# Performance work log

Hardware: AMD Instinct MI355X
Metric: run time of the kernel (lower is better)

The kernel has to match this reference:

```python
import jax, jax.numpy as jnp
import numpy as np

N_HEADS = 4
NUM_GROUPS = 32
EPS = 1e-6


def _nin(t, W, b):
    # 1x1 conv as dense over channel dim: [B,C,H,W] x [C,D] -> [B,D,H,W]
    return jnp.einsum('bchw,cd->bdhw', t, W) + b[None, :, None, None]


def setup_inputs() -> dict:
    key = jax.random.key(0)
    ks = jax.random.split(key, 12)
    B, C, H, W = 8, 256, 32, 32
    Tc = 512
    Cin = C + Tc  # 768
    x = jax.random.normal(ks[0], (B, C, H, W), dtype=jnp.float32)
    text_feat = jax.random.normal(ks[1], (B, Tc), dtype=jnp.float32)
    gn_gamma = jnp.ones((Cin,), dtype=jnp.float32)
    gn_beta = jnp.zeros((Cin,), dtype=jnp.float32)
    scale = 1.0 / np.sqrt(Cin)
    W0 = jax.random.normal(ks[2], (Cin, C), dtype=jnp.float32) * scale
    b0 = jnp.zeros((C,), dtype=jnp.float32)
    W1 = jax.random.normal(ks[3], (Cin, C), dtype=jnp.float32) * scale
    b1 = jnp.zeros((C,), dtype=jnp.float32)
    W2 = jax.random.normal(ks[4], (Cin, C), dtype=jnp.float32) * scale
    b2 = jnp.zeros((C,), dtype=jnp.float32)
    return {"x": x, "text_feat": text_feat, "gn_gamma": gn_gamma, "gn_beta": gn_beta,
            "W0": W0, "b0": b0, "W1": W1, "b1": b1, "W2": W2, "b2": b2}


def reference(x, text_feat, gn_gamma, gn_beta, W0, b0, W1, b1, W2, b2):
    B, C, H, W = x.shape
    # broadcast text features spatially and concat on channel dim
    tf = jnp.broadcast_to(text_feat[:, :, None, None], (B, text_feat.shape[1], H, W))
    h = jnp.concatenate([x, tf], axis=1)  # [B, C+Tc, H, W]
    Ctot = h.shape[1]
    # GroupNorm(32, Ctot), eps=1e-6
    hg = h.reshape(B, NUM_GROUPS, Ctot // NUM_GROUPS, H, W)
    mu = hg.mean(axis=(2, 3, 4), keepdims=True)
    var = hg.var(axis=(2, 3, 4), keepdims=True)
    hn = ((hg - mu) * jax.lax.rsqrt(var + EPS)).reshape(B, Ctot, H, W)
    hn = hn * gn_gamma[None, :, None, None] + gn_beta[None, :, None, None]
    q = _nin(hn, W0, b0)
    k = _nin(hn, W1, b1)
    v = _nin(hn, W2, b2)
    Ch = C // N_HEADS
    qh = q.reshape(B * N_HEADS, Ch, H, W)
    kh = k.reshape(B * N_HEADS, Ch, H, W)
    vh = v.reshape(B * N_HEADS, Ch, H, W)
    # full HW x HW attention scores, softmax over flattened key positions
    w = jnp.einsum('bchw,bcij->bhwij', qh, kh) * (Ch ** -0.5)
    w = jax.nn.softmax(w.reshape(B * N_HEADS, H, W, H * W), axis=-1)
    w = w.reshape(B * N_HEADS, H, W, H, W)
    ho = jnp.einsum('bhwij,bcij->bchw', w, vh).reshape(B, C, H, W)
    return x + ho
```

## Files before the change

### kernel.cpp

```cpp
#include <hip/hip_runtime.h>
#include <math.h>

#define BATCH 8
#define CX 256
#define TC 512
#define CIN 768
#define HW_TOT 1024
#define NH 4
#define CHD 64

typedef __attribute__((ext_vector_type(8))) short short8;
typedef __attribute__((ext_vector_type(4))) short s4v;
typedef __attribute__((ext_vector_type(4))) float floatx4;
typedef __attribute__((ext_vector_type(4))) int int4v;

#define QSCALE 0.18033688f

static __device__ __forceinline__ short f2bf(float f) {
    union { float f; unsigned u; } c; c.f = f;
    unsigned r = (c.u + 0x7fffu + ((c.u >> 16) & 1u)) >> 16;
    return (short)r;
}

static __device__ __forceinline__ int pack_trunc(float lo, float hi) {
    union { float f; unsigned u; } L, H;
    L.f = lo; H.f = hi;
    return (int)((H.u & 0xffff0000u) | (L.u >> 16));
}

__global__ __launch_bounds__(256)
void gn_kernel(const float* __restrict__ x, const float* __restrict__ tf,
               const float* __restrict__ gamma, const float* __restrict__ beta,
               float* __restrict__ scale, float* __restrict__ shift,
               float* __restrict__ tc) {
    const int b = blockIdx.x >> 5;
    const int g = blockIdx.x & 31;
    const int t = threadIdx.x;
    const int w = t >> 6, lane = t & 63;
    if (blockIdx.x < 24) tc[blockIdx.x * 256 + t] = 0.f;

    float s = 0.f, ss = 0.f;
    #pragma unroll
    for (int rr = 0; rr < 6; rr++) {
        const int row = w * 6 + rr;
        const int cg = g * 24 + row;
        if (cg < CX) {
            const float4* p = (const float4*)(x + ((size_t)b * CX + cg) * HW_TOT);
            #pragma unroll
            for (int i = 0; i < 4; i++) {
                float4 v = p[lane + 64 * i];
                s += v.x + v.y + v.z + v.w;
                ss += v.x * v.x + v.y * v.y + v.z * v.z + v.w * v.w;
            }
        } else {
            float v = tf[b * TC + cg - CX];
            s += 16.f * v;
            ss += 16.f * v * v;
        }
    }
    #pragma unroll
    for (int d = 1; d < 64; d <<= 1) {
        s += __shfl_xor(s, d);
        ss += __shfl_xor(ss, d);
    }
    __shared__ float rs_[4], rss_[4];
    if (lane == 0) { rs_[w] = s; rss_[w] = ss; }
    __syncthreads();
    const float S  = rs_[0] + rs_[1] + rs_[2] + rs_[3];
    const float SS = rss_[0] + rss_[1] + rss_[2] + rss_[3];
    const float inv_n = 1.f / (24 * 1024);
    const float mean = S * inv_n;
    const float var = SS * inv_n - mean * mean;
    const float r = rsqrtf(var + 1e-6f);
    if (t < 24) {
        int cg = g * 24 + t;
        float sc = gamma[cg] * r;
        scale[b * CIN + cg] = sc;
        shift[b * CIN + cg] = beta[cg] - mean * sc;
    }
}

__global__ __launch_bounds__(256)
void prep_kernel(const float* __restrict__ x, const float* __restrict__ tf,
                 const float* __restrict__ scale, const float* __restrict__ shift,
                 const float* __restrict__ W0, const float* __restrict__ W1,
                 const float* __restrict__ W2,
                 short* __restrict__ hnT, short* __restrict__ Wt,
                 float* __restrict__ tc) {
    __shared__ float hs[128];
    __shared__ float red[4][64];
    const int bx = blockIdx.x;
    const int t = threadIdx.x;
    if (bx < 256) {
        int id = (bx & 31) * 256 + t;
        int b = id >> 10;
        const float* xb = x + (size_t)b * CX * HW_TOT + (id & 1023);
        const float* scb = scale + b * CIN;
        const float* shb = shift + b * CIN;
        short* outp = hnT + (size_t)id * CX;
        int c0base = (bx >> 5) * 32;
        for (int c0 = c0base; c0 < c0base + 32; c0 += 8) {
            short8 o;
            #pragma unroll
            for (int i = 0; i < 8; i++) {
                float v = xb[(size_t)(c0 + i) * HW_TOT];
                o[i] = f2bf(v * scb[c0 + i] + shb[c0 + i]);
            }
            *(short8*)(outp + c0) = o;
        }
    } else if (bx < 268) {
        int m = bx - 256;
        int dg = (m % 3) * 256 + t;
        int which = dg >> 8, d = dg & 255;
        const float* Wm = (which == 0) ? W0 : (which == 1) ? W1 : W2;
        int c0base = (m / 3) * 64;
        for (int c0 = c0base; c0 < c0base + 64; c0 += 8) {
            short8 o;
            #pragma unroll
            for (int i = 0; i < 8; i++) o[i] = f2bf(Wm[(size_t)(c0 + i) * CX + d]);
            *(short8*)(Wt + (size_t)dg * CX + c0) = o;
        }
    } else {
        int m = bx - 268;
        int ks = m & 3;
        int b = (m >> 2) & 7, dt = m >> 5;
        int which = dt >> 2, d0 = (dt & 3) * 64;
        const float* Wm = (which == 0) ? W0 : (which == 1) ? W1 : W2;
        if (t < 128) {
            int c = ks * 128 + t;
            hs[t] = tf[b * TC + c] * scale[b * CIN + CX + c] + shift[b * CIN + CX + c];
        }
        __syncthreads();
        int td = t & 63, tq = t >> 6;
        float acc = 0.f;
        const float* wp = Wm + (size_t)(CX + ks * 128 + tq * 32) * CX + d0 + td;
        #pragma unroll 8
        for (int c = 0; c < 32; c++)
            acc = fmaf(hs[tq * 32 + c], wp[(size_t)c * CX], acc);
        red[tq][td] = acc;
        __syncthreads();
        if (t < 64)
            atomicAdd(&tc[b * CIN + which * CX + d0 + t],
                      red[0][t] + red[1][t] + red[2][t] + red[3][t]);
    }
}

__global__ __launch_bounds__(256)
void qkv_gemm(const short* __restrict__ hnT, const short* __restrict__ Wt,
              const float* __restrict__ tc,
              const float* __restrict__ b0, const float* __restrict__ b1,
              const float* __restrict__ b2,
              short* __restrict__ qb, short* __restrict__ kb, short* __restrict__ vb) {
    const int hw0 = blockIdx.x * 64, dt = blockIdx.y, b = blockIdx.z;
    const int which = dt >> 2;
    const int col0 = (dt & 3) * 64;
    const int dg0 = which * 256 + col0;
    const bool OV = (which == 2);

    __shared__ short At[64 * 72];
    __shared__ short Bt[64 * 72];

    const int t = threadIdx.x;
    const int w = t >> 6, l = t & 63;
    const int wm = w >> 1, wn = w & 1;
    const int l15 = l & 15, q = l >> 4;
    const int srow = t >> 2, sch = (t & 3) * 16;

    const short* gA = hnT + (size_t)(b * HW_TOT + hw0 + srow) * CX + sch;
    const short* gB = Wt + (size_t)(dg0 + srow) * CX + sch;

    floatx4 acc[2][2] = {};
    for (int k0 = 0; k0 < CX; k0 += 64) {
        __syncthreads();
        *(short8*)(At + srow * 72 + sch)     = *(const short8*)(gA + k0);
        *(short8*)(At + srow * 72 + sch + 8) = *(const short8*)(gA + k0 + 8);
        *(short8*)(Bt + srow * 72 + sch)     = *(const short8*)(gB + k0);
        *(short8*)(Bt + srow * 72 + sch + 8) = *(const short8*)(gB + k0 + 8);
        __syncthreads();
        const short* aB = OV ? Bt : At;
        const short* bB = OV ? At : Bt;
        #pragma unroll
        for (int kc = 0; kc < 2; kc++) {
            short8 af[2], bf2[2];
            #pragma unroll
            for (int mt = 0; mt < 2; mt++)
                af[mt] = *(const short8*)(aB + (wm * 32 + mt * 16 + l15) * 72 + kc * 32 + q * 8);
            #pragma unroll
            for (int nt = 0; nt < 2; nt++)
                bf2[nt] = *(const short8*)(bB + (wn * 32 + nt * 16 + l15) * 72 + kc * 32 + q * 8);
            #pragma unroll
            for (int mt = 0; mt < 2; mt++)
                #pragma unroll
                for (int nt = 0; nt < 2; nt++)
                    acc[mt][nt] = __builtin_amdgcn_mfma_f32_16x16x32_bf16(
                        af[mt], bf2[nt], acc[mt][nt], 0, 0, 0);
        }
    }

    __syncthreads();
    const float* bias = (which == 0) ? b0 : (which == 1) ? b1 : b2;
    if (!OV) {
        const float qs = (which == 0) ? QSCALE : 1.0f;
        float cadd[2];
        #pragma unroll
        for (int nt = 0; nt < 2; nt++) {
            int d = col0 + wn * 32 + nt * 16 + l15;
            cadd[nt] = bias[d] + tc[b * CIN + which * CX + d];
        }
        #pragma unroll
        for (int mt = 0; mt < 2; mt++)
            #pragma unroll
            for (int rr = 0; rr < 4; rr++)
                #pragma unroll
                for (int nt = 0; nt < 2; nt++)
                    At[(wm * 32 + mt * 16 + q * 4 + rr) * 72 + wn * 32 + nt * 16 + l15]
                        = f2bf((acc[mt][nt][rr] + cadd[nt]) * qs);
    } else {
        #pragma unroll
        for (int mt = 0; mt < 2; mt++)
            #pragma unroll
            for (int rr = 0; rr < 4; rr++) {
                int d = col0 + wm * 32 + mt * 16 + q * 4 + rr;
                float radd = bias[d] + tc[b * CIN + 2 * CX + d];
                #pragma unroll
                for (int nt = 0; nt < 2; nt++)
                    At[(wm * 32 + mt * 16 + q * 4 + rr) * 72 + wn * 32 + nt * 16 + l15]
                        = f2bf(acc[mt][nt][rr] + radd);
            }
    }
    __syncthreads();
    short8 v0 = *(const short8*)(At + srow * 72 + sch);
    short8 v1 = *(const short8*)(At + srow * 72 + sch + 8);
    if (!OV) {
        short* outp = (which == 0) ? qb : kb;
        size_t off = (size_t)(b * HW_TOT + hw0 + srow) * CX + col0 + sch;
        *(short8*)(outp + off) = v0;
        *(short8*)(outp + off + 8) = v1;
    } else {
        size_t off = (size_t)(b * CX + col0 + srow) * HW_TOT + hw0 + sch;
        *(short8*)(vb + off) = v0;
        *(short8*)(vb + off + 8) = v1;
    }
}

__global__ __launch_bounds__(256)
void attn_kernel(const short* __restrict__ qb, const short* __restrict__ kb,
                 const short* __restrict__ vb, const float* __restrict__ x,
                 float* __restrict__ out) {
    const int qt = blockIdx.x, bh = blockIdx.y;
    const int b = bh >> 2, h = bh & 3;
    const int hw0 = qt * 128;

    __shared__ short Qs[128 * 72];
    __shared__ short Ks[2][64 * 72];
    __shared__ short Vs[2][64 * 72];

    const int t = threadIdx.x;
    const int w = t >> 6, l = t & 63;
    const int l15 = l & 15, q = l >> 4;
    const int srow = t >> 2, sch = (t & 3) * 16;
    const int vpos0 = ((sch >> 5) << 5) + ((sch >> 4) & 1) * 4;

    {
        #pragma unroll
        for (int rr = 0; rr < 2; rr++) {
            const short* gq = qb + (size_t)(b * HW_TOT + hw0 + rr * 64 + srow) * CX
                            + h * CHD + sch;
            *(short8*)(Qs + (rr * 64 + srow) * 72 + sch)     = *(const short8*)gq;
            *(short8*)(Qs + (rr * 64 + srow) * 72 + sch + 8) = *(const short8*)(gq + 8);
        }
    }

    short8 pk0, pk1, pv0, pv1;
    {
        const short* gk = kb + (size_t)(b * HW_TOT + 0 + srow) * CX + h * CHD + sch;
        pk0 = *(const short8*)gk;
        pk1 = *(const short8*)(gk + 8);
        const short* gv = vb + (size_t)(b * CX + h * CHD + srow) * HW_TOT + 0 + sch;
        pv0 = *(const short8*)gv;
        pv1 = *(const short8*)(gv + 8);
        *(short8*)(Ks[0] + srow * 72 + sch)     = pk0;
        *(short8*)(Ks[0] + srow * 72 + sch + 8) = pk1;
        short* vrow = Vs[0] + srow * 72 + vpos0;
        *(s4v*)(vrow)      = __builtin_shufflevector(pv0, pv0, 0, 1, 2, 3);
        *(s4v*)(vrow + 8)  = __builtin_shufflevector(pv0, pv0, 4, 5, 6, 7);
        *(s4v*)(vrow + 16) = __builtin_shufflevector(pv1, pv1, 0, 1, 2, 3);
        *(s4v*)(vrow + 24) = __builtin_shufflevector(pv1, pv1, 4, 5, 6, 7);
    }
    __syncthreads();

    short8 aq[2][2];
    #pragma unroll
    for (int g = 0; g < 2; g++) {
        aq[g][0] = *(const short8*)(Qs + (w * 32 + g * 16 + l15) * 72 + q * 8);
        aq[g][1] = *(const short8*)(Qs + (w * 32 + g * 16 + l15) * 72 + 32 + q * 8);
    }

    union { int4v i; short8 s; } ones;
    ones.i[0] = 0x3f803f80; ones.i[1] = 0x3f803f80;
    ones.i[2] = 0x3f803f80; ones.i[3] = 0x3f803f80;

    floatx4 oacc[2][4] = {};
    floatx4 lacc[2] = {};

    for (int jj = 0; jj < 16; jj++) {
        const int cur = jj & 1;
        if (jj < 15) {
            const int j0 = (jj + 1) * 64;
            const short* gk = kb + (size_t)(b * HW_TOT + j0 + srow) * CX + h * CHD + sch;
            pk0 = *(const short8*)gk;
            pk1 = *(const short8*)(gk + 8);
            const short* gv = vb + (size_t)(b * CX + h * CHD + srow) * HW_TOT + j0 + sch;
            pv0 = *(const short8*)gv;
            pv1 = *(const short8*)(gv + 8);
        }

        const short* Kc = Ks[cur];
        floatx4 sacc[2][4] = {};
        #pragma unroll
        for (int nt = 0; nt < 4; nt++) {
            short8 kf0 = *(const short8*)(Kc + (nt * 16 + l15) * 72 + q * 8);
            short8 kf1 = *(const short8*)(Kc + (nt * 16 + l15) * 72 + 32 + q * 8);
            #pragma unroll
            for (int g = 0; g < 2; g++) {
                sacc[g][nt] = __builtin_amdgcn_mfma_f32_16x16x32_bf16(kf0, aq[g][0], sacc[g][nt], 0, 0, 0);
                sacc[g][nt] = __builtin_amdgcn_mfma_f32_16x16x32_bf16(kf1, aq[g][1], sacc[g][nt], 0, 0, 0);
            }
        }

        union { int4v i; short8 s; } u[2][2];
        #pragma unroll
        for (int g = 0; g < 2; g++)
            #pragma unroll
            for (int nt = 0; nt < 4; nt++) {
                float e0 = exp2f(sacc[g][nt][0]);
                float e1 = exp2f(sacc[g][nt][1]);
                float e2 = exp2f(sacc[g][nt][2]);
                float e3 = exp2f(sacc[g][nt][3]);
                u[g][nt >> 1].i[(nt & 1) * 2]     = pack_trunc(e0, e1);
                u[g][nt >> 1].i[(nt & 1) * 2 + 1] = pack_trunc(e2, e3);
            }

        #pragma unroll
        for (int g = 0; g < 2; g++) {
            lacc[g] = __builtin_amdgcn_mfma_f32_16x16x32_bf16(ones.s, u[g][0].s, lacc[g], 0, 0, 0);
            lacc[g] = __builtin_amdgcn_mfma_f32_16x16x32_bf16(ones.s, u[g][1].s, lacc[g], 0, 0, 0);
        }

        const short* Vc = Vs[cur];
        #pragma unroll
        for (int ct = 0; ct < 4; ct++) {
            const short* vr = Vc + (ct * 16 + l15) * 72;
            #pragma unroll
            for (int kcc = 0; kcc < 2; kcc++) {
                short8 vf = *(const short8*)(vr + kcc * 32 + q * 8);
                #pragma unroll
                for (int g = 0; g < 2; g++)
                    oacc[g][ct] = __builtin_amdgcn_mfma_f32_16x16x32_bf16(
                        vf, u[g][kcc].s, oacc[g][ct], 0, 0, 0);
            }
        }

        if (jj < 15) {
            __syncthreads();
            *(short8*)(Ks[1 - cur] + srow * 72 + sch)     = pk0;
            *(short8*)(Ks[1 - cur] + srow * 72 + sch + 8) = pk1;
            short* vrow = Vs[1 - cur] + srow * 72 + vpos0;
            *(s4v*)(vrow)      = __builtin_shufflevector(pv0, pv0, 0, 1, 2, 3);
            *(s4v*)(vrow + 8)  = __builtin_shufflevector(pv0, pv0, 4, 5, 6, 7);
            *(s4v*)(vrow + 16) = __builtin_shufflevector(pv1, pv1, 0, 1, 2, 3);
            *(s4v*)(vrow + 24) = __builtin_shufflevector(pv1, pv1, 4, 5, 6, 7);
            __syncthreads();
        }
    }

    #pragma unroll
    for (int g = 0; g < 2; g++) {
        const float rinv = 1.f / lacc[g][0];
        #pragma unroll
        for (int ct = 0; ct < 4; ct++)
            #pragma unroll
            for (int r = 0; r < 4; r++) {
                int c = h * CHD + ct * 16 + q * 4 + r;
                size_t idx = (size_t)(b * CX + c) * HW_TOT + hw0 + w * 32 + g * 16 + l15;
                out[idx] = x[idx] + oacc[g][ct][r] * rinv;
            }
    }
}

extern "C" void kernel_launch(void* const* d_in, const int* in_sizes, int n_in,
                              void* d_out, int out_size, void* d_ws, size_t ws_size,
                              hipStream_t stream) {
    (void)in_sizes; (void)n_in; (void)out_size; (void)ws_size;
    const float* x     = (const float*)d_in[0];
    const float* tf    = (const float*)d_in[1];
    const float* gamma = (const float*)d_in[2];
    const float* beta  = (const float*)d_in[3];
    const float* W0 = (const float*)d_in[4];
    const float* b0 = (const float*)d_in[5];
    const float* W1 = (const float*)d_in[6];
    const float* b1 = (const float*)d_in[7];
    const float* W2 = (const float*)d_in[8];
    const float* b2 = (const float*)d_in[9];

    char* ws = (char*)d_ws;
    float* scale  = (float*)(ws);
    float* shift  = (float*)(ws + 24576);
    float* tcb    = (float*)(ws + 49152);
    short* Wt     = (short*)(ws + 73728);
    short* hnT    = (short*)(ws + 466944);
    short* qb     = (short*)(ws + 4661248);
    short* kb     = (short*)(ws + 8855552);
    short* vb     = (short*)(ws + 13049856);

    hipLaunchKernelGGL(gn_kernel, dim3(256), dim3(256), 0, stream,
                       x, tf, gamma, beta, scale, shift, tcb);
    hipLaunchKernelGGL(prep_kernel, dim3(652), dim3(256), 0, stream,
                       x, tf, scale, shift, W0, W1, W2, hnT, Wt, tcb);
    hipLaunchKernelGGL(qkv_gemm, dim3(16, 12, BATCH), dim3(256), 0, stream,
                       hnT, Wt, tcb, b0, b1, b2, qb, kb, vb);
    hipLaunchKernelGGL(attn_kernel, dim3(8, 32), dim3(256), 0, stream,
                       qb, kb, vb, x, (float*)d_out);
}
```

Measured before the change: 124.9 us.

## Split attention key range across wave pairs and halve query tile per block

The attention kernel now handles 64 queries per block instead of 128, which doubles the grid to 512 blocks. Within a block, two wave pairs each process one half of the key sequence (a split-K style scheme) and merge their partial outputs and row sums through shared memory at the end. The intent is more blocks and more parallelism to fill the CUs, plus a launch-bounds occupancy hint. The cost is a doubled K/V load per query, with each K/V tile now read by twice as many blocks, and an extra shared-memory reduction. Dropping the per-tile double buffering also exposes some load latency.

```diff
diff --git a/kernel.cpp b/kernel.cpp
--- a/kernel.cpp
+++ b/kernel.cpp
@@ -243,57 +243,59 @@
     }
 }
 
-__global__ __launch_bounds__(256)
+__global__ __launch_bounds__(256, 3)
 void attn_kernel(const short* __restrict__ qb, const short* __restrict__ kb,
                  const short* __restrict__ vb, const float* __restrict__ x,
                  float* __restrict__ out) {
     const int qt = blockIdx.x, bh = blockIdx.y;
     const int b = bh >> 2, h = bh & 3;
-    const int hw0 = qt * 128;
-
-    __shared__ short Qs[128 * 72];
+    const int hw0 = qt * 64;
+
+    __shared__ short Qs[64 * 72];
     __shared__ short Ks[2][64 * 72];
     __shared__ short Vs[2][64 * 72];
 
     const int t = threadIdx.x;
     const int w = t >> 6, l = t & 63;
+    const int pair = w >> 1, jh = w & 1;
     const int l15 = l & 15, q = l >> 4;
     const int srow = t >> 2, sch = (t & 3) * 16;
     const int vpos0 = ((sch >> 5) << 5) + ((sch >> 4) & 1) * 4;
 
     {
-        #pragma unroll
-        for (int rr = 0; rr < 2; rr++) {
-            const short* gq = qb + (size_t)(b * HW_TOT + hw0 + rr * 64 + srow) * CX
-                            + h * CHD + sch;
-            *(short8*)(Qs + (rr * 64 + srow) * 72 + sch)     = *(const short8*)gq;
-            *(short8*)(Qs + (rr * 64 + srow) * 72 + sch + 8) = *(const short8*)(gq + 8);
-        }
-    }
-
-    short8 pk0, pk1, pv0, pv1;
-    {
-        const short* gk = kb + (size_t)(b * HW_TOT + 0 + srow) * CX + h * CHD + sch;
-        pk0 = *(const short8*)gk;
-        pk1 = *(const short8*)(gk + 8);
-        const short* gv = vb + (size_t)(b * CX + h * CHD + srow) * HW_TOT + 0 + sch;
-        pv0 = *(const short8*)gv;
-        pv1 = *(const short8*)(gv + 8);
-        *(short8*)(Ks[0] + srow * 72 + sch)     = pk0;
-        *(short8*)(Ks[0] + srow * 72 + sch + 8) = pk1;
-        short* vrow = Vs[0] + srow * 72 + vpos0;
-        *(s4v*)(vrow)      = __builtin_shufflevector(pv0, pv0, 0, 1, 2, 3);
-        *(s4v*)(vrow + 8)  = __builtin_shufflevector(pv0, pv0, 4, 5, 6, 7);
-        *(s4v*)(vrow + 16) = __builtin_shufflevector(pv1, pv1, 0, 1, 2, 3);
-        *(s4v*)(vrow + 24) = __builtin_shufflevector(pv1, pv1, 4, 5, 6, 7);
+        const short* gq = qb + (size_t)(b * HW_TOT + hw0 + srow) * CX + h * CHD + sch;
+        *(short8*)(Qs + srow * 72 + sch)     = *(const short8*)gq;
+        *(short8*)(Qs + srow * 72 + sch + 8) = *(const short8*)(gq + 8);
+    }
+
+    short8 pk[2][2], pv[2][2];
+    #pragma unroll
+    for (int s = 0; s < 2; s++) {
+        const int j0 = s * 512;
+        const short* gk = kb + (size_t)(b * HW_TOT + j0 + srow) * CX + h * CHD + sch;
+        pk[s][0] = *(const short8*)gk;
+        pk[s][1] = *(const short8*)(gk + 8);
+        const short* gv = vb + (size_t)(b * CX + h * CHD + srow) * HW_TOT + j0 + sch;
+        pv[s][0] = *(const short8*)gv;
+        pv[s][1] = *(const short8*)(gv + 8);
+    }
+    #pragma unroll
+    for (int s = 0; s < 2; s++) {
+        *(short8*)(Ks[s] + srow * 72 + sch)     = pk[s][0];
+        *(short8*)(Ks[s] + srow * 72 + sch + 8) = pk[s][1];
+        short* vrow = Vs[s] + srow * 72 + vpos0;
+        *(s4v*)(vrow)      = __builtin_shufflevector(pv[s][0], pv[s][0], 0, 1, 2, 3);
+        *(s4v*)(vrow + 8)  = __builtin_shufflevector(pv[s][0], pv[s][0], 4, 5, 6, 7);
+        *(s4v*)(vrow + 16) = __builtin_shufflevector(pv[s][1], pv[s][1], 0, 1, 2, 3);
+        *(s4v*)(vrow + 24) = __builtin_shufflevector(pv[s][1], pv[s][1], 4, 5, 6, 7);
     }
     __syncthreads();
 
     short8 aq[2][2];
     #pragma unroll
     for (int g = 0; g < 2; g++) {
-        aq[g][0] = *(const short8*)(Qs + (w * 32 + g * 16 + l15) * 72 + q * 8);
-        aq[g][1] = *(const short8*)(Qs + (w * 32 + g * 16 + l15) * 72 + 32 + q * 8);
+        aq[g][0] = *(const short8*)(Qs + (pair * 32 + g * 16 + l15) * 72 + q * 8);
+        aq[g][1] = *(const short8*)(Qs + (pair * 32 + g * 16 + l15) * 72 + 32 + q * 8);
     }
 
     union { int4v i; short8 s; } ones;
@@ -302,20 +304,23 @@
 
     floatx4 oacc[2][4] = {};
     floatx4 lacc[2] = {};
-
-    for (int jj = 0; jj < 16; jj++) {
-        const int cur = jj & 1;
-        if (jj < 15) {
-            const int j0 = (jj + 1) * 64;
-            const short* gk = kb + (size_t)(b * HW_TOT + j0 + srow) * CX + h * CHD + sch;
-            pk0 = *(const short8*)gk;
-            pk1 = *(const short8*)(gk + 8);
-            const short* gv = vb + (size_t)(b * CX + h * CHD + srow) * HW_TOT + j0 + sch;
-            pv0 = *(const short8*)gv;
-            pv1 = *(const short8*)(gv + 8);
-        }
-
-        const short* Kc = Ks[cur];
+    const short* Kc = Ks[jh];
+    const short* Vc = Vs[jh];
+
+    for (int jj = 0; jj < 8; jj++) {
+        if (jj < 7) {
+            #pragma unroll
+            for (int s = 0; s < 2; s++) {
+                const int j0 = s * 512 + (jj + 1) * 64;
+                const short* gk = kb + (size_t)(b * HW_TOT + j0 + srow) * CX + h * CHD + sch;
+                pk[s][0] = *(const short8*)gk;
+                pk[s][1] = *(const short8*)(gk + 8);
+                const short* gv = vb + (size_t)(b * CX + h * CHD + srow) * HW_TOT + j0 + sch;
+                pv[s][0] = *(const short8*)gv;
+                pv[s][1] = *(const short8*)(gv + 8);
+            }
+        }
+
         floatx4 sacc[2][4] = {};
         #pragma unroll
         for (int nt = 0; nt < 4; nt++) {
@@ -347,7 +352,6 @@
             lacc[g] = __builtin_amdgcn_mfma_f32_16x16x32_bf16(ones.s, u[g][1].s, lacc[g], 0, 0, 0);
         }
 
-        const short* Vc = Vs[cur];
         #pragma unroll
         for (int ct = 0; ct < 4; ct++) {
             const short* vr = Vc + (ct * 16 + l15) * 72;
@@ -361,30 +365,52 @@
             }
         }
 
-        if (jj < 15) {
+        if (jj < 7) {
             __syncthreads();
-            *(short8*)(Ks[1 - cur] + srow * 72 + sch)     = pk0;
-            *(short8*)(Ks[1 - cur] + srow * 72 + sch + 8) = pk1;
-            short* vrow = Vs[1 - cur] + srow * 72 + vpos0;
-            *(s4v*)(vrow)      = __builtin_shufflevector(pv0, pv0, 0, 1, 2, 3);
-            *(s4v*)(vrow + 8)  = __builtin_shufflevector(pv0, pv0, 4, 5, 6, 7);
-            *(s4v*)(vrow + 16) = __builtin_shufflevector(pv1, pv1, 0, 1, 2, 3);
-            *(s4v*)(vrow + 24) = __builtin_shufflevector(pv1, pv1, 4, 5, 6, 7);
+            #pragma unroll
+            for (int s = 0; s < 2; s++) {
+                *(short8*)(Ks[s] + srow * 72 + sch)     = pk[s][0];
+                *(short8*)(Ks[s] + srow * 72 + sch + 8) = pk[s][1];
+                short* vrow = Vs[s] + srow * 72 + vpos0;
+                *(s4v*)(vrow)      = __builtin_shufflevector(pv[s][0], pv[s][0], 0, 1, 2, 3);
+                *(s4v*)(vrow + 8)  = __builtin_shufflevector(pv[s][0], pv[s][0], 4, 5, 6, 7);
+                *(s4v*)(vrow + 16) = __builtin_shufflevector(pv[s][1], pv[s][1], 0, 1, 2, 3);
+                *(s4v*)(vrow + 24) = __builtin_shufflevector(pv[s][1], pv[s][1], 4, 5, 6, 7);
+            }
             __syncthreads();
         }
     }
 
-    #pragma unroll
-    for (int g = 0; g < 2; g++) {
-        const float rinv = 1.f / lacc[g][0];
-        #pragma unroll
-        for (int ct = 0; ct < 4; ct++)
-            #pragma unroll
-            for (int r = 0; r < 4; r++) {
-                int c = h * CHD + ct * 16 + q * 4 + r;
-                size_t idx = (size_t)(b * CX + c) * HW_TOT + hw0 + w * 32 + g * 16 + l15;
-                out[idx] = x[idx] + oacc[g][ct][r] * rinv;
-            }
+    __syncthreads();
+    float* Of = (float*)Ks;
+    float* Lf = (float*)Vs;
+    if (jh == 1) {
+        #pragma unroll
+        for (int g = 0; g < 2; g++) {
+            int qi = pair * 32 + g * 16 + l15;
+            #pragma unroll
+            for (int ct = 0; ct < 4; ct++)
+                *(floatx4*)&Of[qi * 68 + ct * 16 + q * 4] = oacc[g][ct];
+            if (q == 0) Lf[qi] = lacc[g][0];
+        }
+    }
+    __syncthreads();
+    if (jh == 0) {
+        #pragma unroll
+        for (int g = 0; g < 2; g++) {
+            int qi = pair * 32 + g * 16 + l15;
+            const float rinv = 1.f / (lacc[g][0] + Lf[qi]);
+            #pragma unroll
+            for (int ct = 0; ct < 4; ct++) {
+                floatx4 po = *(const floatx4*)&Of[qi * 68 + ct * 16 + q * 4];
+                #pragma unroll
+                for (int r = 0; r < 4; r++) {
+                    int c = h * CHD + ct * 16 + q * 4 + r;
+                    size_t idx = (size_t)(b * CX + c) * HW_TOT + hw0 + qi;
+                    out[idx] = x[idx] + (oacc[g][ct][r] + po[r]) * rinv;
+                }
+            }
+        }
     }
 }
 
@@ -419,6 +445,6 @@
                        x, tf, scale, shift, W0, W1, W2, hnT, Wt, tcb);
     hipLaunchKernelGGL(qkv_gemm, dim3(16, 12, BATCH), dim3(256), 0, stream,
                        hnT, Wt, tcb, b0, b1, b2, qb, kb, vb);
-    hipLaunchKernelGGL(attn_kernel, dim3(8, 32), dim3(256), 0, stream,
+    hipLaunchKernelGGL(attn_kernel, dim3(16, 32), dim3(256), 0, stream,
                        qb, kb, vb, x, (float*)d_out);
 }
```

Result: faster. 118.6 us (-5.1%).
